# Optimization experiments

Hardware: AMD Instinct MI355X
Metric: run time of the kernel (lower is better)

Reference implementation:

```python
import jax, jax.numpy as jnp
import numpy as np

NUM_USERS = 100000
NUM_ITEMS = 50000
EMB_DIM = 64
NUM_LAYERS = 3
NUM_EDGES = 1000000


def _xavier(key, shape):
    fan_in, fan_out = shape[-1], shape[-2] if len(shape) > 1 else shape[-1]
    limit = float(np.sqrt(6.0 / (fan_in + fan_out)))
    return jax.random.uniform(key, shape, jnp.float32, -limit, limit)


def setup_inputs() -> dict:
    key = jax.random.key(0)
    ks = jax.random.split(key, 8)
    edge_u = jax.random.randint(ks[0], (NUM_EDGES,), 0, NUM_USERS)
    edge_i = jax.random.randint(ks[1], (NUM_EDGES,), 0, NUM_ITEMS)
    u_emb = _xavier(ks[2], (NUM_USERS, EMB_DIM))
    i_emb = _xavier(ks[3], (NUM_ITEMS, EMB_DIM))
    Wgc = _xavier(ks[4], (NUM_LAYERS, EMB_DIM, EMB_DIM))
    Wbi = _xavier(ks[5], (NUM_LAYERS, EMB_DIM, EMB_DIM))
    bgc = jnp.zeros((NUM_LAYERS, EMB_DIM), jnp.float32)
    bbi = jnp.zeros((NUM_LAYERS, EMB_DIM), jnp.float32)
    return {"u_emb": u_emb, "i_emb": i_emb, "Wgc": Wgc, "bgc": bgc,
            "Wbi": Wbi, "bbi": bbi, "edge_u": edge_u, "edge_i": edge_i}


def _smooth(X, src, dst, dv_isqrt, de_inv, num_v, num_e):
    # HGNN smoothing: D_v^{-1/2} H D_e^{-1} H^T D_v^{-1/2} X via edge list
    X1 = X * dv_isqrt[:, None]
    E = jax.ops.segment_sum(X1[src], dst, num_segments=num_e) * de_inv[:, None]
    Y = jax.ops.segment_sum(E[dst], src, num_segments=num_v)
    return Y * dv_isqrt[:, None]


def reference(u_emb, i_emb, Wgc, bgc, Wbi, bbi, edge_u, edge_i):
    NU, NI, D = u_emb.shape[0], i_emb.shape[0], u_emb.shape[1]
    ones = jnp.ones((edge_u.shape[0],), jnp.float32)
    deg_u = jax.ops.segment_sum(ones, edge_u, num_segments=NU)
    deg_i = jax.ops.segment_sum(ones, edge_i, num_segments=NI)
    du_isqrt = jnp.where(deg_u > 0, deg_u, 1.0) ** -0.5 * (deg_u > 0)
    di_isqrt = jnp.where(deg_i > 0, deg_i, 1.0) ** -0.5 * (deg_i > 0)
    du_inv = jnp.where(deg_u > 0, 1.0 / jnp.where(deg_u > 0, deg_u, 1.0), 0.0)
    di_inv = jnp.where(deg_i > 0, 1.0 / jnp.where(deg_i > 0, deg_i, 1.0), 0.0)

    all_embs = jnp.concatenate([u_emb, i_emb], axis=0)
    embs_list = [all_embs]
    for l in range(Wgc.shape[0]):
        u, i = all_embs[:NU], all_embs[NU:]
        # hg_ui: users = vertices, items = hyperedges
        u_s = _smooth(u, edge_u, edge_i, du_isqrt, di_inv, NU, NI)
        # hg_iu: items = vertices, users = hyperedges
        i_s = _smooth(i, edge_i, edge_u, di_isqrt, du_inv, NI, NU)
        g = jnp.concatenate([u_s, i_s], axis=0)
        sum_embs = jax.nn.leaky_relu(g @ Wgc[l].T + bgc[l] + all_embs, negative_slope=0.2)
        bi_embs = jax.nn.leaky_relu((all_embs * g) @ Wbi[l].T + bbi[l], negative_slope=0.2)
        all_embs = sum_embs + bi_embs  # dropout off (eval mode)
        norm = jnp.sqrt(jnp.sum(all_embs * all_embs, axis=1, keepdims=True))
        all_embs = all_embs / jnp.maximum(norm, 1e-12)
        embs_list.append(all_embs)
    embs = jnp.mean(jnp.stack(embs_list, axis=1), axis=1)
    return embs[:NU], embs[NU:]
```

## Files before the change

kernel.cpp:

```cpp
#include <hip/hip_runtime.h>
#include <cstdint>
#include <cstddef>

#define NU 100000
#define NI 50000
#define NTOT 150000
#define EDIM 64
#define NE 1000000
#define NLAYERS 3
#define NTILES (NTOT / 16)
#define NPAIR (NTOT / 2)

#define NBKT 256
#define NPB 586
#define NSHARD 8
#define BCAP 1920
#define BCUR_STRIDE 16
#define BIN_EPB 1024
#define BIN_NBLK ((NE + BIN_EPB - 1) / BIN_EPB)
#define SLICE_CAP 13312

typedef __attribute__((ext_vector_type(8))) short short8;
typedef __attribute__((ext_vector_type(4))) float floatx4;

__device__ inline unsigned short f2bf(float f) {
    unsigned u = __float_as_uint(f);
    u += 0x7fffu + ((u >> 16) & 1u);
    return (unsigned short)(u >> 16);
}
__device__ inline unsigned pack_bf2(float a, float b) {
    unsigned ua = __float_as_uint(a); ua += 0x7fffu + ((ua >> 16) & 1u);
    unsigned ub = __float_as_uint(b); ub += 0x7fffu + ((ub >> 16) & 1u);
    return (ua >> 16) | (ub & 0xffff0000u);
}
__device__ inline float bf_lo(unsigned u) { return __uint_as_float(u << 16); }
__device__ inline float bf_hi(unsigned u) { return __uint_as_float(u & 0xffff0000u); }

__global__ __launch_bounds__(256) void k_binpairs(const int* __restrict__ eu,
                                                  const int* __restrict__ ei,
                                                  unsigned* __restrict__ bcur,
                                                  uint2* __restrict__ bbuf) {
    int shard = blockIdx.x & (NSHARD - 1);
    int ebase = blockIdx.x * BIN_EPB + threadIdx.x;
    int n_[8], o_[8];
#pragma unroll
    for (int k = 0; k < 4; ++k) {
        int e = ebase + k * 256;
        int u = (e < NE) ? eu[e] : -1;
        int v = (e < NE) ? NU + ei[e] : -1;
        n_[k] = u;     o_[k] = v;
        n_[k + 4] = v; o_[k + 4] = u;
    }
    int bb_[8];
#pragma unroll
    for (int k = 0; k < 8; ++k) bb_[k] = (n_[k] >= 0) ? (n_[k] / NPB) : -1;
    int pp_[8];
#pragma unroll
    for (int k = 0; k < 8; ++k)
        pp_[k] = (bb_[k] >= 0)
                     ? (int)atomicAdd(&bcur[(bb_[k] * NSHARD + shard) * BCUR_STRIDE], 1u)
                     : -1;
#pragma unroll
    for (int k = 0; k < 8; ++k)
        if (pp_[k] >= 0 && pp_[k] < BCAP)
            bbuf[(size_t)(bb_[k] * NSHARD + shard) * BCAP + pp_[k]] =
                make_uint2((unsigned)n_[k], (unsigned)o_[k]);
}

__global__ void k_bktprefix(const unsigned* __restrict__ bcur, int* __restrict__ bktbase) {
    __shared__ int sm[256];
    int t = threadIdx.x;
    int tot = 0;
    for (int s = 0; s < NSHARD; ++s) tot += (int)bcur[(t * NSHARD + s) * BCUR_STRIDE];
    sm[t] = tot;
    __syncthreads();
    for (int off = 1; off < 256; off <<= 1) {
        int tmp = (t >= off) ? sm[t - off] : 0;
        __syncthreads();
        sm[t] += tmp;
        __syncthreads();
    }
    bktbase[t] = sm[t] - tot;
}

__global__ __launch_bounds__(1024) void k_buildcsr(
    const uint2* __restrict__ bbuf, const unsigned* __restrict__ bcur,
    const int* __restrict__ bktbase, int* __restrict__ deg, int* __restrict__ start,
    float* __restrict__ isq, float* __restrict__ inv, int* __restrict__ csr) {
    __shared__ int slice[SLICE_CAP];
    __shared__ int lcur[NPB];
    __shared__ int scnt[NSHARD];
    int b = blockIdx.x;
    int t = threadIdx.x;
    int n0 = b * NPB;
    int nn = NTOT - n0;
    if (nn > NPB) nn = NPB;
    if (nn < 0) nn = 0;
    if (t < NPB) lcur[t] = 0;
    if (t < NSHARD) {
        int c = (int)bcur[(b * NSHARD + t) * BCUR_STRIDE];
        scnt[t] = c < BCAP ? c : BCAP;
    }
    __syncthreads();
    for (int s = 0; s < NSHARD; ++s) {
        int c = scnt[s];
        const uint2* pb = bbuf + (size_t)(b * NSHARD + s) * BCAP;
        for (int i = t; i < c; i += 1024) atomicAdd(&lcur[(int)pb[i].x - n0], 1);
    }
    __syncthreads();
    int cnt_t = (t < nn) ? lcur[t] : 0;
    slice[t] = cnt_t;
    __syncthreads();
    for (int off = 1; off < 1024; off <<= 1) {
        int tmp = (t >= off) ? slice[t - off] : 0;
        __syncthreads();
        slice[t] += tmp;
        __syncthreads();
    }
    int excl = slice[t] - cnt_t;
    int slen = slice[1023];
    int bb = bktbase[b];
    if (t < nn) {
        int n = n0 + t;
        deg[n] = cnt_t;
        start[n] = bb + excl;
        float df = (float)cnt_t;
        isq[n] = cnt_t > 0 ? 1.0f / sqrtf(df) : 0.f;
        inv[n] = cnt_t > 0 ? 1.0f / df : 0.f;
    }
    __syncthreads();
    if (t < nn) lcur[t] = excl;
    __syncthreads();
    for (int s = 0; s < NSHARD; ++s) {
        int c = scnt[s];
        const uint2* pb = bbuf + (size_t)(b * NSHARD + s) * BCAP;
        for (int i = t; i < c; i += 1024) {
            uint2 pr = pb[i];
            int idx = atomicAdd(&lcur[(int)pr.x - n0], 1);
            if (idx < SLICE_CAP) slice[idx] = (int)pr.y;
        }
    }
    __syncthreads();
    if (slen > SLICE_CAP) slen = SLICE_CAP;
    for (int i = t; i < slen; i += 1024) csr[bb + i] = slice[i];
}

__global__ void k_init(const float* __restrict__ ue, const float* __restrict__ ie,
                       const float* __restrict__ isq,
                       unsigned* __restrict__ snap0, unsigned* gbuf,
                       const float* __restrict__ Wg, const float* __restrict__ Wb,
                       unsigned short* __restrict__ wgb, unsigned short* __restrict__ wbb,
                       unsigned* __restrict__ Ebuf) {
    int i = blockIdx.x * blockDim.x + threadIdx.x;
    const int n4 = NTOT * EDIM / 4;
    const int nw4 = NLAYERS * 4096 / 4;
    if (i < nw4) {
        float4 g4 = ((const float4*)Wg)[i];
        float4 b4 = ((const float4*)Wb)[i];
        uint2 g, b;
        g.x = pack_bf2(g4.x, g4.y); g.y = pack_bf2(g4.z, g4.w);
        b.x = pack_bf2(b4.x, b4.y); b.y = pack_bf2(b4.z, b4.w);
        ((uint2*)wgb)[i] = g;
        ((uint2*)wbb)[i] = b;
    }
    if (i < 16) {
        ((uint2*)(Ebuf + NTOT * 32))[i] = make_uint2(0u, 0u);
        ((uint2*)(gbuf + NTOT * 32))[i] = make_uint2(0u, 0u);
    }
    if (i < n4) {
        const int nu4 = NU * EDIM / 4;
        float4 v = (i < nu4) ? ((const float4*)ue)[i] : ((const float4*)ie)[i - nu4];
        float s = isq[i >> 4];
        uint2 b, bs;
        b.x = pack_bf2(v.x, v.y);
        b.y = pack_bf2(v.z, v.w);
        bs.x = pack_bf2(v.x * s, v.y * s);
        bs.y = pack_bf2(v.z * s, v.w * s);
        ((uint2*)snap0)[i] = b;
        ((uint2*)gbuf)[i] = bs;
    }
}

__global__ __launch_bounds__(256) void k_gather(
    const unsigned* __restrict__ in_bf, unsigned* __restrict__ out_bf,
    const int* __restrict__ csr, const int* __restrict__ start,
    const int* __restrict__ deg, const float* __restrict__ sA) {
    int gw = (blockIdx.x * 256 + threadIdx.x) >> 6;
    int lane = threadIdx.x & 63;
    if (gw >= NPAIR) return;
    int l2 = lane & 31;
    int hbase = lane & 32;
    int row = gw * 2 + (lane >> 5);
    int s0 = start[row];
    int dg = deg[row];
    int dgo = __shfl_xor(dg, 32);
    int dgmax = max(dg, dgo);
    float acc0 = 0.f, acc1 = 0.f;
    for (int j0 = 0; j0 < dgmax; j0 += 32) {
        int nidx = NTOT;
        if (j0 + l2 < dg) nidx = csr[s0 + j0 + l2];
        int jlim = min(32, dgmax - j0);
        for (int j = 0; j < jlim; j += 16) {
            int mm[16];
            unsigned uu[16];
#pragma unroll
            for (int k = 0; k < 16; ++k)
                mm[k] = __shfl(nidx, hbase + j + k);
#pragma unroll
            for (int k = 0; k < 16; ++k)
                uu[k] = in_bf[mm[k] * 32 + l2];
#pragma unroll
            for (int k = 0; k < 16; ++k) {
                acc0 += bf_lo(uu[k]);
                acc1 += bf_hi(uu[k]);
            }
        }
    }
    float s = sA[row];
    out_bf[row * 32 + l2] = pack_bf2(s * acc0, s * acc1);
}

__global__ __launch_bounds__(256) void k_dense_mfma(
    const unsigned short* __restrict__ a_prev, unsigned* gbuf,
    unsigned short* __restrict__ snap_l, const float* __restrict__ isq,
    const unsigned short* __restrict__ wgb, const unsigned short* __restrict__ wbb,
    const float* __restrict__ bg, const float* __restrict__ bb, int writeScaled,
    int finalOut, const unsigned short* __restrict__ s1,
    const float* __restrict__ ue, const float* __restrict__ ie,
    float* __restrict__ outp) {
    int lane = threadIdx.x & 63;
    int lanelo = lane & 15;
    int quad = lane >> 4;
    int wid = (blockIdx.x * blockDim.x + threadIdx.x) >> 6;
    if (wid >= NTILES) return;

    short8 bWg[4][2], bWb[4][2];
#pragma unroll
    for (int t = 0; t < 4; ++t) {
#pragma unroll
        for (int h = 0; h < 2; ++h) {
            int n = t * 16 + lanelo;
            int k0 = h * 32 + quad * 8;
            bWg[t][h] = *(const short8*)&wgb[n * 64 + k0];
            bWb[t][h] = *(const short8*)&wbb[n * 64 + k0];
        }
    }
    float bgv[4], bbv[4];
#pragma unroll
    for (int t = 0; t < 4; ++t) {
        bgv[t] = bg[t * 16 + lanelo];
        bbv[t] = bb[t * 16 + lanelo];
    }

    int rbase = wid * 16;
    int arow = rbase + lanelo;
    short8 aG[2], aAG[2];
#pragma unroll
    for (int h = 0; h < 2; ++h) {
        uint4 ug = *(const uint4*)(gbuf + arow * 32 + h * 16 + quad * 4);
        uint4 ua = *(const uint4*)((const unsigned*)a_prev + arow * 32 + h * 16 + quad * 4);
        aG[h] = *(const short8*)&ug;
        uint4 up;
        up.x = pack_bf2(bf_lo(ua.x) * bf_lo(ug.x), bf_hi(ua.x) * bf_hi(ug.x));
        up.y = pack_bf2(bf_lo(ua.y) * bf_lo(ug.y), bf_hi(ua.y) * bf_hi(ug.y));
        up.z = pack_bf2(bf_lo(ua.z) * bf_lo(ug.z), bf_hi(ua.z) * bf_hi(ug.z));
        up.w = pack_bf2(bf_lo(ua.w) * bf_lo(ug.w), bf_hi(ua.w) * bf_hi(ug.w));
        aAG[h] = *(const short8*)&up;
    }
    floatx4 accg[4], accb[4];
#pragma unroll
    for (int t = 0; t < 4; ++t) {
        accg[t] = (floatx4)(0.f);
        accb[t] = (floatx4)(0.f);
    }
#pragma unroll
    for (int t = 0; t < 4; ++t) {
#pragma unroll
        for (int h = 0; h < 2; ++h) {
            accg[t] = __builtin_amdgcn_mfma_f32_16x16x32_bf16(aG[h], bWg[t][h], accg[t], 0, 0, 0);
            accb[t] = __builtin_amdgcn_mfma_f32_16x16x32_bf16(aAG[h], bWb[t][h], accb[t], 0, 0, 0);
        }
    }
    float nv[4][4];
    float ss[4] = {0.f, 0.f, 0.f, 0.f};
#pragma unroll
    for (int i = 0; i < 4; ++i) {
        int r = rbase + quad * 4 + i;
#pragma unroll
        for (int t = 0; t < 4; ++t) {
            float a = __uint_as_float((unsigned)a_prev[r * 64 + t * 16 + lanelo] << 16);
            float e1 = accg[t][i] + bgv[t] + a;
            e1 = e1 >= 0.f ? e1 : 0.2f * e1;
            float e2 = accb[t][i] + bbv[t];
            e2 = e2 >= 0.f ? e2 : 0.2f * e2;
            float v = e1 + e2;
            nv[i][t] = v;
            ss[i] += v * v;
        }
    }
#pragma unroll
    for (int m = 1; m < 16; m <<= 1) {
#pragma unroll
        for (int i = 0; i < 4; ++i) ss[i] += __shfl_xor(ss[i], m, 64);
    }
#pragma unroll
    for (int i = 0; i < 4; ++i) {
        int r = rbase + quad * 4 + i;
        float rn = 1.0f / fmaxf(sqrtf(ss[i]), 1e-12f);
        float sc = isq[r] * rn;
        if (finalOut) {
#pragma unroll
            for (int t = 0; t < 4; ++t) {
                int idx = r * 64 + t * 16 + lanelo;
                float rr = nv[i][t] * rn;
                float s1v = __uint_as_float((unsigned)s1[idx] << 16);
                float s2v = __uint_as_float((unsigned)a_prev[idx] << 16);
                float ev = (r < NU) ? ue[idx] : ie[idx - NU * 64];
                outp[idx] = 0.25f * (ev + s1v + s2v + rr);
            }
        } else {
#pragma unroll
            for (int t = 0; t < 4; ++t) {
                int idx = r * 64 + t * 16 + lanelo;
                float rr = nv[i][t] * rn;
                snap_l[idx] = f2bf(rr);
                if (writeScaled)
                    ((unsigned short*)gbuf)[idx] = f2bf(nv[i][t] * sc);
            }
        }
    }
}


extern "C" void kernel_launch(void* const* d_in, const int* in_sizes, int n_in,
                              void* d_out, int out_size, void* d_ws, size_t ws_size,
                              hipStream_t stream) {
    const float* u_emb = (const float*)d_in[0];
    const float* i_emb = (const float*)d_in[1];
    const float* Wgc = (const float*)d_in[2];
    const float* bgc = (const float*)d_in[3];
    const float* Wbi = (const float*)d_in[4];
    const float* bbi = (const float*)d_in[5];
    const int* edge_u = (const int*)d_in[6];
    const int* edge_i = (const int*)d_in[7];
    float* out = (float*)d_out;

    char* w = (char*)d_ws;
    auto alloc = [&](size_t bytes) {
        char* p = w;
        w += (bytes + 255) & ~(size_t)255;
        return p;
    };
    const size_t ROWBYTES = (size_t)(NTOT + 1) * EDIM * 2;
    int* deg = (int*)alloc((size_t)NTOT * 4);
    int* start = (int*)alloc((size_t)NTOT * 4);
    unsigned* bcur = (unsigned*)alloc((size_t)NBKT * NSHARD * BCUR_STRIDE * 4);
    int* bktbase = (int*)alloc(256 * 4);
    int* csr = (int*)alloc((size_t)2 * NE * 4);
    float* isq = (float*)alloc((size_t)NTOT * 4);
    float* inv = (float*)alloc((size_t)NTOT * 4);
    unsigned short* wgb = (unsigned short*)alloc((size_t)NLAYERS * 4096 * 2);
    unsigned short* wbb = (unsigned short*)alloc((size_t)NLAYERS * 4096 * 2);
    unsigned* snap0 = (unsigned*)alloc((size_t)NTOT * EDIM * 2);
    unsigned* snap1 = (unsigned*)alloc((size_t)NTOT * EDIM * 2);
    unsigned* snap2 = (unsigned*)alloc((size_t)NTOT * EDIM * 2);
    unsigned* Ebuf = (unsigned*)alloc(ROWBYTES);
    unsigned* gbuf = (unsigned*)alloc(ROWBYTES);
    uint2* bbuf = (uint2*)snap1;

    hipMemsetAsync(bcur, 0, (size_t)NBKT * NSHARD * BCUR_STRIDE * 4, stream);
    k_binpairs<<<BIN_NBLK, 256, 0, stream>>>(edge_u, edge_i, bcur, bbuf);
    k_bktprefix<<<1, 256, 0, stream>>>(bcur, bktbase);
    k_buildcsr<<<NBKT, 1024, 0, stream>>>(bbuf, bcur, bktbase, deg, start, isq, inv, csr);
    k_init<<<(NTOT * EDIM / 4 + 255) / 256, 256, 0, stream>>>(
        u_emb, i_emb, isq, snap0, gbuf, Wgc, Wbi, wgb, wbb, Ebuf);

    const int gatherBlocks = (NPAIR * 64 + 255) / 256;
    const int denseBlocks = (NTILES * 64 + 255) / 256;
    const unsigned short* aprev[3] = {(unsigned short*)snap0, (unsigned short*)snap1,
                                      (unsigned short*)snap2};
    unsigned short* snaps[3] = {(unsigned short*)snap1, (unsigned short*)snap2,
                                (unsigned short*)snap1 };
    for (int l = 0; l < NLAYERS; ++l) {
        k_gather<<<gatherBlocks, 256, 0, stream>>>(gbuf, Ebuf, csr, start, deg, inv);
        k_gather<<<gatherBlocks, 256, 0, stream>>>(Ebuf, gbuf, csr, start, deg, isq);
        k_dense_mfma<<<denseBlocks, 256, 0, stream>>>(
            aprev[l], gbuf, snaps[l], isq, wgb + (size_t)l * 4096, wbb + (size_t)l * 4096,
            bgc + (size_t)l * 64, bbi + (size_t)l * 64,
            l < NLAYERS - 1 ? 1 : 0,
            l == NLAYERS - 1 ? 1 : 0,
            (const unsigned short*)snap1, u_emb, i_emb, out);
    }
}
```

Measured before the change: 535.9 us.

## Stage edge binning in shared memory and pack pairs into single words

```diff
diff --git a/kernel.cpp b/kernel.cpp
--- a/kernel.cpp
+++ b/kernel.cpp
@@ -13,11 +13,13 @@
 
 #define NBKT 256
 #define NPB 586
-#define NSHARD 8
-#define BCAP 1920
+#define NSHARD 1
+#define BCAP 13312
 #define BCUR_STRIDE 16
 #define BIN_EPB 1024
 #define BIN_NBLK ((NE + BIN_EPB - 1) / BIN_EPB)
+#define LCAP 28
+#define LPAD 29
 #define SLICE_CAP 13312
 
 typedef __attribute__((ext_vector_type(8))) short short8;
@@ -39,39 +41,53 @@
 __global__ __launch_bounds__(256) void k_binpairs(const int* __restrict__ eu,
                                                   const int* __restrict__ ei,
                                                   unsigned* __restrict__ bcur,
-                                                  uint2* __restrict__ bbuf) {
-    int shard = blockIdx.x & (NSHARD - 1);
-    int ebase = blockIdx.x * BIN_EPB + threadIdx.x;
-    int n_[8], o_[8];
+                                                  unsigned* __restrict__ bbuf) {
+    __shared__ unsigned lbuf[NBKT * LPAD];
+    __shared__ int lcnt[NBKT];
+    int t = threadIdx.x;
+    if (t < NBKT) lcnt[t] = 0;
+    __syncthreads();
+    int ebase = blockIdx.x * BIN_EPB + t;
 #pragma unroll
     for (int k = 0; k < 4; ++k) {
         int e = ebase + k * 256;
-        int u = (e < NE) ? eu[e] : -1;
-        int v = (e < NE) ? NU + ei[e] : -1;
-        n_[k] = u;     o_[k] = v;
-        n_[k + 4] = v; o_[k + 4] = u;
-    }
-    int bb_[8];
-#pragma unroll
-    for (int k = 0; k < 8; ++k) bb_[k] = (n_[k] >= 0) ? (n_[k] / NPB) : -1;
-    int pp_[8];
-#pragma unroll
-    for (int k = 0; k < 8; ++k)
-        pp_[k] = (bb_[k] >= 0)
-                     ? (int)atomicAdd(&bcur[(bb_[k] * NSHARD + shard) * BCUR_STRIDE], 1u)
-                     : -1;
-#pragma unroll
-    for (int k = 0; k < 8; ++k)
-        if (pp_[k] >= 0 && pp_[k] < BCAP)
-            bbuf[(size_t)(bb_[k] * NSHARD + shard) * BCAP + pp_[k]] =
-                make_uint2((unsigned)n_[k], (unsigned)o_[k]);
+        if (e < NE) {
+            int u = eu[e];
+            int v = NU + ei[e];
+            int b0 = u / NPB;
+            int w0 = ((u - b0 * NPB) << 18) | v;
+            int p0 = atomicAdd(&lcnt[b0], 1);
+            if (p0 < LCAP) lbuf[b0 * LPAD + p0] = (unsigned)w0;
+            else {
+                unsigned gp = atomicAdd(&bcur[b0 * BCUR_STRIDE], 1u);
+                if (gp < BCAP) bbuf[(size_t)b0 * BCAP + gp] = (unsigned)w0;
+            }
+            int b1 = v / NPB;
+            int w1 = ((v - b1 * NPB) << 18) | u;
+            int p1 = atomicAdd(&lcnt[b1], 1);
+            if (p1 < LCAP) lbuf[b1 * LPAD + p1] = (unsigned)w1;
+            else {
+                unsigned gp = atomicAdd(&bcur[b1 * BCUR_STRIDE], 1u);
+                if (gp < BCAP) bbuf[(size_t)b1 * BCAP + gp] = (unsigned)w1;
+            }
+        }
+    }
+    __syncthreads();
+    int nb = min(lcnt[t], LCAP);
+    if (nb > 0) {
+        unsigned gp = atomicAdd(&bcur[t * BCUR_STRIDE], (unsigned)nb);
+        for (int i = 0; i < nb; ++i) {
+            unsigned idx = gp + i;
+            if (idx < BCAP) bbuf[(size_t)t * BCAP + idx] = lbuf[t * LPAD + i];
+        }
+    }
 }
 
 __global__ void k_bktprefix(const unsigned* __restrict__ bcur, int* __restrict__ bktbase) {
     __shared__ int sm[256];
     int t = threadIdx.x;
-    int tot = 0;
-    for (int s = 0; s < NSHARD; ++s) tot += (int)bcur[(t * NSHARD + s) * BCUR_STRIDE];
+    int tot = (int)bcur[t * BCUR_STRIDE];
+    if (tot > BCAP) tot = BCAP;
     sm[t] = tot;
     __syncthreads();
     for (int off = 1; off < 256; off <<= 1) {
@@ -84,12 +100,12 @@
 }
 
 __global__ __launch_bounds__(1024) void k_buildcsr(
-    const uint2* __restrict__ bbuf, const unsigned* __restrict__ bcur,
+    const unsigned* __restrict__ bbuf, const unsigned* __restrict__ bcur,
     const int* __restrict__ bktbase, int* __restrict__ deg, int* __restrict__ start,
     float* __restrict__ isq, float* __restrict__ inv, int* __restrict__ csr) {
     __shared__ int slice[SLICE_CAP];
     __shared__ int lcur[NPB];
-    __shared__ int scnt[NSHARD];
+    __shared__ int scnt_s;
     int b = blockIdx.x;
     int t = threadIdx.x;
     int n0 = b * NPB;
@@ -97,16 +113,14 @@
     if (nn > NPB) nn = NPB;
     if (nn < 0) nn = 0;
     if (t < NPB) lcur[t] = 0;
-    if (t < NSHARD) {
-        int c = (int)bcur[(b * NSHARD + t) * BCUR_STRIDE];
-        scnt[t] = c < BCAP ? c : BCAP;
-    }
-    __syncthreads();
-    for (int s = 0; s < NSHARD; ++s) {
-        int c = scnt[s];
-        const uint2* pb = bbuf + (size_t)(b * NSHARD + s) * BCAP;
-        for (int i = t; i < c; i += 1024) atomicAdd(&lcur[(int)pb[i].x - n0], 1);
-    }
+    if (t == 0) {
+        int c = (int)bcur[b * BCUR_STRIDE];
+        scnt_s = c < BCAP ? c : BCAP;
+    }
+    __syncthreads();
+    int c = scnt_s;
+    const unsigned* pb = bbuf + (size_t)b * BCAP;
+    for (int i = t; i < c; i += 1024) atomicAdd(&lcur[(int)(pb[i] >> 18)], 1);
     __syncthreads();
     int cnt_t = (t < nn) ? lcur[t] : 0;
     slice[t] = cnt_t;
@@ -131,14 +145,10 @@
     __syncthreads();
     if (t < nn) lcur[t] = excl;
     __syncthreads();
-    for (int s = 0; s < NSHARD; ++s) {
-        int c = scnt[s];
-        const uint2* pb = bbuf + (size_t)(b * NSHARD + s) * BCAP;
-        for (int i = t; i < c; i += 1024) {
-            uint2 pr = pb[i];
-            int idx = atomicAdd(&lcur[(int)pr.x - n0], 1);
-            if (idx < SLICE_CAP) slice[idx] = (int)pr.y;
-        }
+    for (int i = t; i < c; i += 1024) {
+        unsigned pr = pb[i];
+        int idx = atomicAdd(&lcur[(int)(pr >> 18)], 1);
+        if (idx < SLICE_CAP) slice[idx] = (int)(pr & 0x3FFFFu);
     }
     __syncthreads();
     if (slen > SLICE_CAP) slen = SLICE_CAP;
@@ -354,7 +364,7 @@
     const size_t ROWBYTES = (size_t)(NTOT + 1) * EDIM * 2;
     int* deg = (int*)alloc((size_t)NTOT * 4);
     int* start = (int*)alloc((size_t)NTOT * 4);
-    unsigned* bcur = (unsigned*)alloc((size_t)NBKT * NSHARD * BCUR_STRIDE * 4);
+    unsigned* bcur = (unsigned*)alloc((size_t)NBKT * BCUR_STRIDE * 4);
     int* bktbase = (int*)alloc(256 * 4);
     int* csr = (int*)alloc((size_t)2 * NE * 4);
     float* isq = (float*)alloc((size_t)NTOT * 4);
@@ -366,9 +376,9 @@
     unsigned* snap2 = (unsigned*)alloc((size_t)NTOT * EDIM * 2);
     unsigned* Ebuf = (unsigned*)alloc(ROWBYTES);
     unsigned* gbuf = (unsigned*)alloc(ROWBYTES);
-    uint2* bbuf = (uint2*)snap1;
-
-    hipMemsetAsync(bcur, 0, (size_t)NBKT * NSHARD * BCUR_STRIDE * 4, stream);
+    unsigned* bbuf = (unsigned*)snap1;
+
+    hipMemsetAsync(bcur, 0, (size_t)NBKT * BCUR_STRIDE * 4, stream);
     k_binpairs<<<BIN_NBLK, 256, 0, stream>>>(edge_u, edge_i, bcur, bbuf);
     k_bktprefix<<<1, 256, 0, stream>>>(bcur, bktbase);
     k_buildcsr<<<NBKT, 1024, 0, stream>>>(bbuf, bcur, bktbase, deg, start, isq, inv, csr);
```

Result: faster. 468.4 us (-12.6%).
